# Optimization experiments

Measured on AMD Instinct MI355X. Metric: run time of the kernel, lower is better.

The kernel has to match this reference:

```python
import jax, jax.numpy as jnp
import numpy as np

BETA = 0.9
THRESH = 1.0
SLOPE = 25.0  # snntorch fast_sigmoid default slope
T = 4096

@jax.custom_vjp
def spike_fn(x):
    # Heaviside forward, fast-sigmoid surrogate backward
    return (x > 0).astype(x.dtype)

def _spike_fwd(x):
    return (x > 0).astype(x.dtype), x

def _spike_bwd(x, g):
    return (g / (SLOPE * jnp.abs(x) + 1.0) ** 2,)

spike_fn.defvjp(_spike_fwd, _spike_bwd)

def setup_inputs():
    key = jax.random.key(0)
    ks = jax.random.split(key, 5)
    B = 1024
    x = jax.random.normal(ks[0], (B, 6, T), dtype=jnp.float32)
    W1 = jax.random.normal(ks[1], (10, 6), dtype=jnp.float32) / np.sqrt(6.0)
    b1 = jax.random.normal(ks[2], (10,), dtype=jnp.float32) * 0.01
    W2 = jax.random.normal(ks[3], (27, 10), dtype=jnp.float32) / np.sqrt(10.0)
    b2 = jax.random.normal(ks[4], (27,), dtype=jnp.float32) * 0.01
    return {"x": x, "W1": W1, "b1": b1, "W2": W2, "b2": b2}

def reference(x, W1, b1, W2, b2):
    B = x.shape[0]
    xt = jnp.transpose(x, (2, 0, 1))  # [T, B, 6]
    mem1_0 = jnp.zeros((B, 10), x.dtype)
    mem2_0 = jnp.zeros((B, 27), x.dtype)

    def step(carry, xin):
        mem1, mem2 = carry
        cur1 = xin @ W1.T + b1                              # [B,10]
        rst1 = jax.lax.stop_gradient((mem1 > THRESH).astype(x.dtype))
        mem1 = BETA * mem1 + cur1 - rst1 * THRESH           # subtract reset
        spk1 = spike_fn(mem1 - THRESH)
        cur2 = spk1 @ W2.T + b2                             # [B,27]
        rst2 = jax.lax.stop_gradient((mem2 > THRESH).astype(x.dtype))
        mem2 = BETA * mem2 + cur2 - rst2 * THRESH
        return (mem1, mem2), None

    (mem1, mem2), _ = jax.lax.scan(step, (mem1_0, mem2_0), xt)
    # module returns only the spike of the final timestep
    return spike_fn(mem2 - THRESH)
```

## Files before the change

### kernel.cpp

```cpp
#include <hip/hip_runtime.h>


#define T_STEPS 4096
#define BETA 0.9f
#define THRESH 1.0f
#define CH 64
#define NCHUNK (T_STEPS / CH)
#define GRP 8
#define NGRP (CH / GRP)

__global__ __launch_bounds__(192, 1) void snn_kernel(
    const float* __restrict__ x,
    const float* __restrict__ W1,
    const float* __restrict__ b1,
    const float* __restrict__ W2,
    const float* __restrict__ b2,
    float* __restrict__ out)
{
    __shared__ float tabLo[32 * 32];
    __shared__ float tabHi[32 * 32];
    __shared__ float curBuf[10 * 68];
    __shared__ unsigned maskBuf[2][64];
    __shared__ float cur2Buf[2][27 * 68];

    const int tid = threadIdx.x;
    const int wid = tid >> 6;
    const int l   = tid & 63;
    const int b   = blockIdx.x;

    if (tid < 32) {
        for (int j = 0; j < 27; ++j) {
            float slo = b2[j];
            float shi = 0.0f;
            #pragma unroll
            for (int i = 0; i < 5; ++i) {
                if (tid & (1 << i)) {
                    slo += W2[j * 10 + i];
                    shi += W2[j * 10 + 5 + i];
                }
            }
            tabLo[tid * 32 + j] = slo;
            tabHi[tid * 32 + j] = shi;
        }
    }

    float w1r[60], b1r[10];
    float xv[6], xn[6];
    float mem1 = 0.0f;
    bool  sp1 = false;
    const int ri = (l < 10) ? l : 9;
    const float* cp = &curBuf[ri * 68];
    const float* xb = x + (size_t)b * 6 * T_STEPS;

    if (wid == 0) {
        #pragma unroll
        for (int i = 0; i < 10; ++i) {
            b1r[i] = b1[i];
            #pragma unroll
            for (int c = 0; c < 6; ++c) w1r[i * 6 + c] = W1[i * 6 + c];
        }
        #pragma unroll
        for (int c = 0; c < 6; ++c) xv[c] = xb[c * T_STEPS + l];
    }

    const int gh = l >> 5;
    const int gjr = l & 31;
    const int gj = (gjr < 27) ? gjr : 26;

    float mem2 = 0.0f;
    bool  sp2 = false;
    const int rj = (l < 27) ? l : 26;

    __syncthreads();

    #pragma unroll 1
    for (int k = 0; k <= NCHUNK + 1; ++k) {
        if (wid == 0 && k < NCHUNK) {
            #pragma unroll
            for (int i = 0; i < 10; ++i) {
                float acc = xv[0] * w1r[i * 6 + 0];
                acc = fmaf(xv[1], w1r[i * 6 + 1], acc);
                acc = fmaf(xv[2], w1r[i * 6 + 2], acc);
                acc = fmaf(xv[3], w1r[i * 6 + 3], acc);
                acc = fmaf(xv[4], w1r[i * 6 + 4], acc);
                acc = fmaf(xv[5], w1r[i * 6 + 5], acc);
                curBuf[i * 68 + l] = acc + b1r[i];
            }
            if (k + 1 < NCHUNK) {
                #pragma unroll
                for (int c = 0; c < 6; ++c) xn[c] = xb[c * T_STEPS + (k + 1) * CH + l];
            }

            unsigned vmask = 0u;
            float c1v[8];
            {
                float4 q0 = *(const float4*)(cp + 0);
                float4 q1 = *(const float4*)(cp + 4);
                c1v[0] = q0.x; c1v[1] = q0.y; c1v[2] = q0.z; c1v[3] = q0.w;
                c1v[4] = q1.x; c1v[5] = q1.y; c1v[6] = q1.z; c1v[7] = q1.w;
            }
            #pragma unroll
            for (int g = 0; g < NGRP; ++g) {
                float c1n[8];
                if (g + 1 < NGRP) {
                    float4 p0 = *(const float4*)(cp + (g + 1) * 8);
                    float4 p1 = *(const float4*)(cp + (g + 1) * 8 + 4);
                    c1n[0] = p0.x; c1n[1] = p0.y; c1n[2] = p0.z; c1n[3] = p0.w;
                    c1n[4] = p1.x; c1n[5] = p1.y; c1n[6] = p1.z; c1n[7] = p1.w;
                }
                #pragma unroll
                for (int s = 0; s < 8; ++s) {
                    float t1 = fmaf(BETA, mem1, c1v[s]);
                    mem1 = sp1 ? (t1 - THRESH) : t1;
                    sp1 = mem1 > THRESH;
                    unsigned m = (unsigned)__ballot(sp1);
                    vmask = (l == g * 8 + s) ? m : vmask;
                }
                if (g + 1 < NGRP) {
                    #pragma unroll
                    for (int s = 0; s < 8; ++s) c1v[s] = c1n[s];
                }
            }
            maskBuf[k & 1][l] = vmask;

            if (k + 1 < NCHUNK) {
                #pragma unroll
                for (int c = 0; c < 6; ++c) xv[c] = xn[c];
            }
        }

        if (wid == 1 && k >= 1 && k <= NCHUNK) {
            const int par = (k - 1) & 1;
            const unsigned* mrow = &maskBuf[par][gh];
            float* crow = &cur2Buf[par][gj * 68 + gh];

            unsigned mr[32];
            #pragma unroll
            for (int r = 0; r < 32; ++r) mr[r] = mrow[2 * r];
            #pragma unroll
            for (int r = 0; r < 32; ++r) {
                unsigned alo = (mr[r] & 31u) << 5;
                unsigned ahi = ((mr[r] >> 5) & 31u) << 5;
                crow[2 * r] = tabLo[alo + gj] + tabHi[ahi + gj];
            }
        }

        if (wid == 2 && k >= 2) {
            const float* cp2 = &cur2Buf[(k - 2) & 1][rj * 68];
            float c2v[8];
            {
                float4 q0 = *(const float4*)(cp2 + 0);
                float4 q1 = *(const float4*)(cp2 + 4);
                c2v[0] = q0.x; c2v[1] = q0.y; c2v[2] = q0.z; c2v[3] = q0.w;
                c2v[4] = q1.x; c2v[5] = q1.y; c2v[6] = q1.z; c2v[7] = q1.w;
            }
            #pragma unroll
            for (int g = 0; g < NGRP; ++g) {
                float c2n[8];
                if (g + 1 < NGRP) {
                    float4 p0 = *(const float4*)(cp2 + (g + 1) * 8);
                    float4 p1 = *(const float4*)(cp2 + (g + 1) * 8 + 4);
                    c2n[0] = p0.x; c2n[1] = p0.y; c2n[2] = p0.z; c2n[3] = p0.w;
                    c2n[4] = p1.x; c2n[5] = p1.y; c2n[6] = p1.z; c2n[7] = p1.w;
                }
                #pragma unroll
                for (int s = 0; s < 8; ++s) {
                    float t2 = fmaf(BETA, mem2, c2v[s]);
                    mem2 = sp2 ? (t2 - THRESH) : t2;
                    sp2 = mem2 > THRESH;
                }
                if (g + 1 < NGRP) {
                    #pragma unroll
                    for (int s = 0; s < 8; ++s) c2v[s] = c2n[s];
                }
            }
        }

        __syncthreads();
    }

    if (wid == 2 && l < 27) {
        out[b * 27 + l] = sp2 ? 1.0f : 0.0f;
    }
}

extern "C" void kernel_launch(void* const* d_in, const int* in_sizes, int n_in,
                              void* d_out, int out_size, void* d_ws, size_t ws_size,
                              hipStream_t stream) {
    const float* x  = (const float*)d_in[0];
    const float* W1 = (const float*)d_in[1];
    const float* b1 = (const float*)d_in[2];
    const float* W2 = (const float*)d_in[3];
    const float* b2 = (const float*)d_in[4];
    float* out = (float*)d_out;

    const int B = in_sizes[0] / (6 * T_STEPS);
    snn_kernel<<<dim3(B), dim3(192), 0, stream>>>(x, W1, b1, W2, b2, out);
}
```

Measured before the change: 302.3 us.

## Double pipeline interval to 128 steps and transpose layer-2 current buffer

Each barrier interval now covers 128 timesteps instead of 64. The layer-1 wave does two 64-step passes per interval, so the pipeline needs about half as many block-wide barriers. The layer-2 current buffer is transposed to a time-major layout with a 28-float stride, and the table-lookup wave reads masks with vector loads. Several inner loops are kept rolled, which shrinks code but adds loop overhead to the serial recurrence and doubles the shared-memory staging buffers.

After: 414.9 us. +37.3%, slower.

```diff
diff --git a/kernel.cpp b/kernel.cpp
--- a/kernel.cpp
+++ b/kernel.cpp
@@ -4,10 +4,9 @@
 #define T_STEPS 4096
 #define BETA 0.9f
 #define THRESH 1.0f
-#define CH 64
-#define NCHUNK (T_STEPS / CH)
-#define GRP 8
-#define NGRP (CH / GRP)
+#define IV 128
+#define NI (T_STEPS / IV)
+#define NPASS 2
 
 __global__ __launch_bounds__(192, 1) void snn_kernel(
     const float* __restrict__ x,
@@ -17,11 +16,11 @@
     const float* __restrict__ b2,
     float* __restrict__ out)
 {
-    __shared__ float tabLo[32 * 32];
-    __shared__ float tabHi[32 * 32];
+    __shared__ float tabLo[32 * 28];
+    __shared__ float tabHi[32 * 28];
     __shared__ float curBuf[10 * 68];
-    __shared__ unsigned maskBuf[2][64];
-    __shared__ float cur2Buf[2][27 * 68];
+    __shared__ unsigned maskBuf[2][IV];
+    __shared__ float cur2Buf[2][IV * 28];
 
     const int tid = threadIdx.x;
     const int wid = tid >> 6;
@@ -39,8 +38,8 @@
                     shi += W2[j * 10 + 5 + i];
                 }
             }
-            tabLo[tid * 32 + j] = slo;
-            tabHi[tid * 32 + j] = shi;
+            tabLo[tid * 28 + j] = slo;
+            tabHi[tid * 28 + j] = shi;
         }
     }
 
@@ -63,105 +62,121 @@
         for (int c = 0; c < 6; ++c) xv[c] = xb[c * T_STEPS + l];
     }
 
-    const int gh = l >> 5;
+    const int gh  = l >> 5;
     const int gjr = l & 31;
-    const int gj = (gjr < 27) ? gjr : 26;
+    const int gj  = (gjr < 27) ? gjr : 26;
+    const bool hsel = (gh != 0);
 
     float mem2 = 0.0f;
     bool  sp2 = false;
-    const int rj = (l < 27) ? l : 26;
+    const int jc = (l < 27) ? l : 26;
 
     __syncthreads();
 
     #pragma unroll 1
-    for (int k = 0; k <= NCHUNK + 1; ++k) {
-        if (wid == 0 && k < NCHUNK) {
+    for (int ki = 0; ki <= NI + 1; ++ki) {
+        if (wid == 0 && ki < NI) {
+            #pragma unroll 1
+            for (int c = 0; c < NPASS; ++c) {
+                const int p = ki * NPASS + c;
+                if (p + 1 < NI * NPASS) {
+                    #pragma unroll
+                    for (int ch = 0; ch < 6; ++ch)
+                        xn[ch] = xb[ch * T_STEPS + (p + 1) * 64 + l];
+                }
+                #pragma unroll
+                for (int i = 0; i < 10; ++i) {
+                    float acc = xv[0] * w1r[i * 6 + 0];
+                    acc = fmaf(xv[1], w1r[i * 6 + 1], acc);
+                    acc = fmaf(xv[2], w1r[i * 6 + 2], acc);
+                    acc = fmaf(xv[3], w1r[i * 6 + 3], acc);
+                    acc = fmaf(xv[4], w1r[i * 6 + 4], acc);
+                    acc = fmaf(xv[5], w1r[i * 6 + 5], acc);
+                    curBuf[i * 68 + l] = acc + b1r[i];
+                }
+
+                unsigned vmask = 0u;
+                float c1v[8], c1n[8];
+                {
+                    float4 q0 = *(const float4*)(cp + 0);
+                    float4 q1 = *(const float4*)(cp + 4);
+                    c1v[0] = q0.x; c1v[1] = q0.y; c1v[2] = q0.z; c1v[3] = q0.w;
+                    c1v[4] = q1.x; c1v[5] = q1.y; c1v[6] = q1.z; c1v[7] = q1.w;
+                }
+                #pragma unroll 1
+                for (int g = 0; g < 8; ++g) {
+                    if (g < 7) {
+                        float4 q0 = *(const float4*)(cp + (g + 1) * 8);
+                        float4 q1 = *(const float4*)(cp + (g + 1) * 8 + 4);
+                        c1n[0] = q0.x; c1n[1] = q0.y; c1n[2] = q0.z; c1n[3] = q0.w;
+                        c1n[4] = q1.x; c1n[5] = q1.y; c1n[6] = q1.z; c1n[7] = q1.w;
+                    }
+                    const int lg = l - g * 8;
+                    #pragma unroll
+                    for (int s = 0; s < 8; ++s) {
+                        float t1 = fmaf(BETA, mem1, c1v[s]);
+                        mem1 = sp1 ? (t1 - THRESH) : t1;
+                        sp1 = mem1 > THRESH;
+                        unsigned m = (unsigned)__ballot(sp1);
+                        vmask = (lg == s) ? m : vmask;
+                    }
+                    if (g < 7) {
+                        #pragma unroll
+                        for (int s = 0; s < 8; ++s) c1v[s] = c1n[s];
+                    }
+                }
+                maskBuf[ki & 1][c * 64 + l] = vmask;
+
+                if (p + 1 < NI * NPASS) {
+                    #pragma unroll
+                    for (int ch = 0; ch < 6; ++ch) xv[ch] = xn[ch];
+                }
+            }
+        }
+
+        if (wid == 1 && ki >= 1 && ki <= NI) {
+            const int par = (ki - 1) & 1;
+            const unsigned* mrow = maskBuf[par];
+            float* crow = cur2Buf[par];
+
+            #pragma unroll 1
+            for (int bq = 0; bq < 8; ++bq) {
+                uint4 u0 = *(const uint4*)(mrow + 16 * bq + 0);
+                uint4 u1 = *(const uint4*)(mrow + 16 * bq + 4);
+                uint4 u2 = *(const uint4*)(mrow + 16 * bq + 8);
+                uint4 u3 = *(const uint4*)(mrow + 16 * bq + 12);
+                unsigned me[8];
+                me[0] = hsel ? u0.y : u0.x;  me[1] = hsel ? u0.w : u0.z;
+                me[2] = hsel ? u1.y : u1.x;  me[3] = hsel ? u1.w : u1.z;
+                me[4] = hsel ? u2.y : u2.x;  me[5] = hsel ? u2.w : u2.z;
+                me[6] = hsel ? u3.y : u3.x;  me[7] = hsel ? u3.w : u3.z;
+
+                float tl[8], th[8];
+                #pragma unroll
+                for (int r = 0; r < 8; ++r) {
+                    unsigned rl = (me[r] & 31u) * 28u;
+                    unsigned rh = ((me[r] >> 5) & 31u) * 28u;
+                    tl[r] = tabLo[rl + gj];
+                    th[r] = tabHi[rh + gj];
+                }
+                #pragma unroll
+                for (int r = 0; r < 8; ++r) {
+                    crow[(16 * bq + 2 * r + gh) * 28 + gj] = tl[r] + th[r];
+                }
+            }
+        }
+
+        if (wid == 2 && ki >= 2) {
+            const int par = ki & 1;
+            const float* c2p = &cur2Buf[par][jc];
+            float c2v[8], c2n[8];
             #pragma unroll
-            for (int i = 0; i < 10; ++i) {
-                float acc = xv[0] * w1r[i * 6 + 0];
-                acc = fmaf(xv[1], w1r[i * 6 + 1], acc);
-                acc = fmaf(xv[2], w1r[i * 6 + 2], acc);
-                acc = fmaf(xv[3], w1r[i * 6 + 3], acc);
-                acc = fmaf(xv[4], w1r[i * 6 + 4], acc);
-                acc = fmaf(xv[5], w1r[i * 6 + 5], acc);
-                curBuf[i * 68 + l] = acc + b1r[i];
-            }
-            if (k + 1 < NCHUNK) {
-                #pragma unroll
-                for (int c = 0; c < 6; ++c) xn[c] = xb[c * T_STEPS + (k + 1) * CH + l];
-            }
-
-            unsigned vmask = 0u;
-            float c1v[8];
-            {
-                float4 q0 = *(const float4*)(cp + 0);
-                float4 q1 = *(const float4*)(cp + 4);
-                c1v[0] = q0.x; c1v[1] = q0.y; c1v[2] = q0.z; c1v[3] = q0.w;
-                c1v[4] = q1.x; c1v[5] = q1.y; c1v[6] = q1.z; c1v[7] = q1.w;
-            }
-            #pragma unroll
-            for (int g = 0; g < NGRP; ++g) {
-                float c1n[8];
-                if (g + 1 < NGRP) {
-                    float4 p0 = *(const float4*)(cp + (g + 1) * 8);
-                    float4 p1 = *(const float4*)(cp + (g + 1) * 8 + 4);
-                    c1n[0] = p0.x; c1n[1] = p0.y; c1n[2] = p0.z; c1n[3] = p0.w;
-                    c1n[4] = p1.x; c1n[5] = p1.y; c1n[6] = p1.z; c1n[7] = p1.w;
-                }
-                #pragma unroll
-                for (int s = 0; s < 8; ++s) {
-                    float t1 = fmaf(BETA, mem1, c1v[s]);
-                    mem1 = sp1 ? (t1 - THRESH) : t1;
-                    sp1 = mem1 > THRESH;
-                    unsigned m = (unsigned)__ballot(sp1);
-                    vmask = (l == g * 8 + s) ? m : vmask;
-                }
-                if (g + 1 < NGRP) {
-                    #pragma unroll
-                    for (int s = 0; s < 8; ++s) c1v[s] = c1n[s];
-                }
-            }
-            maskBuf[k & 1][l] = vmask;
-
-            if (k + 1 < NCHUNK) {
-                #pragma unroll
-                for (int c = 0; c < 6; ++c) xv[c] = xn[c];
-            }
-        }
-
-        if (wid == 1 && k >= 1 && k <= NCHUNK) {
-            const int par = (k - 1) & 1;
-            const unsigned* mrow = &maskBuf[par][gh];
-            float* crow = &cur2Buf[par][gj * 68 + gh];
-
-            unsigned mr[32];
-            #pragma unroll
-            for (int r = 0; r < 32; ++r) mr[r] = mrow[2 * r];
-            #pragma unroll
-            for (int r = 0; r < 32; ++r) {
-                unsigned alo = (mr[r] & 31u) << 5;
-                unsigned ahi = ((mr[r] >> 5) & 31u) << 5;
-                crow[2 * r] = tabLo[alo + gj] + tabHi[ahi + gj];
-            }
-        }
-
-        if (wid == 2 && k >= 2) {
-            const float* cp2 = &cur2Buf[(k - 2) & 1][rj * 68];
-            float c2v[8];
-            {
-                float4 q0 = *(const float4*)(cp2 + 0);
-                float4 q1 = *(const float4*)(cp2 + 4);
-                c2v[0] = q0.x; c2v[1] = q0.y; c2v[2] = q0.z; c2v[3] = q0.w;
-                c2v[4] = q1.x; c2v[5] = q1.y; c2v[6] = q1.z; c2v[7] = q1.w;
-            }
-            #pragma unroll
-            for (int g = 0; g < NGRP; ++g) {
-                float c2n[8];
-                if (g + 1 < NGRP) {
-                    float4 p0 = *(const float4*)(cp2 + (g + 1) * 8);
-                    float4 p1 = *(const float4*)(cp2 + (g + 1) * 8 + 4);
-                    c2n[0] = p0.x; c2n[1] = p0.y; c2n[2] = p0.z; c2n[3] = p0.w;
-                    c2n[4] = p1.x; c2n[5] = p1.y; c2n[6] = p1.z; c2n[7] = p1.w;
+            for (int s = 0; s < 8; ++s) c2v[s] = c2p[s * 28];
+            #pragma unroll 1
+            for (int g = 0; g < 16; ++g) {
+                if (g < 15) {
+                    #pragma unroll
+                    for (int s = 0; s < 8; ++s) c2n[s] = c2p[((g + 1) * 8 + s) * 28];
                 }
                 #pragma unroll
                 for (int s = 0; s < 8; ++s) {
@@ -169,7 +184,7 @@
                     mem2 = sp2 ? (t2 - THRESH) : t2;
                     sp2 = mem2 > THRESH;
                 }
-                if (g + 1 < NGRP) {
+                if (g < 15) {
                     #pragma unroll
                     for (int s = 0; s < 8; ++s) c2v[s] = c2n[s];
                 }
```
